# Optimization experiments

Hardware: AMD Instinct MI355X
Metric: run time of the kernel (lower is better)

Reference implementation:

```python
import jax, jax.numpy as jnp
import numpy as np

# UMAP a,b fitted offline for spread=5, min_dist=0.001 (curve_fit of 1/(1+a x^(2b)))
ALPHA = 0.1520
BETA = 0.7900
N_NODES = 50000
IN_DIM = 128
HID = 64
OUT_DIM = 2
N_EDGES = 800000


def setup_inputs() -> dict:
    key = jax.random.key(0)
    ks = jax.random.split(key, 8)
    feats = jax.random.normal(ks[0], (N_NODES, IN_DIM), dtype=jnp.float32)
    W1 = jax.random.normal(ks[1], (IN_DIM, HID), dtype=jnp.float32) / np.sqrt(IN_DIM)
    b1 = jnp.zeros((HID,), dtype=jnp.float32)
    W2 = jax.random.normal(ks[2], (HID, OUT_DIM), dtype=jnp.float32) / np.sqrt(HID)
    b2 = jnp.zeros((OUT_DIM,), dtype=jnp.float32)
    edge_index = jax.random.randint(ks[3], (2, N_EDGES), 0, N_NODES, dtype=jnp.int64)
    row_neg = jax.random.randint(ks[4], (N_EDGES,), 0, N_NODES, dtype=jnp.int64)
    col_neg = jax.random.randint(ks[5], (N_EDGES,), 0, N_NODES, dtype=jnp.int64)
    return {"features": feats, "W1": W1, "b1": b1, "W2": W2, "b2": b2,
            "edge_index": edge_index, "row_neg": row_neg, "col_neg": col_neg}


def _gcn_norm(edge_index, n_nodes):
    # add self-loops, symmetric normalization D^-1/2 (A+I) D^-1/2
    loops = jnp.arange(n_nodes, dtype=edge_index.dtype)
    row = jnp.concatenate([edge_index[0], loops])
    col = jnp.concatenate([edge_index[1], loops])
    deg = jax.ops.segment_sum(jnp.ones_like(row, dtype=jnp.float32), row,
                              num_segments=n_nodes)
    dinv = jnp.where(deg > 0, jax.lax.rsqrt(deg), 0.0)
    norm = dinv[row] * dinv[col]  # [E + N]
    return row, col, norm


def _gcn_conv(x, W, b, row, col, norm, n_nodes):
    h = x @ W                      # [N, out]
    msg = h[col] * norm[:, None]   # edge-indexed gather (irregular access)
    agg = jax.ops.segment_sum(msg, row, num_segments=n_nodes)
    return agg + b


def _forward(features, W1, b1, W2, b2, edge_index, row_neg, col_neg):
    n = features.shape[0]
    row, col, norm = _gcn_norm(edge_index, n)
    h = jax.nn.relu(_gcn_conv(features, W1, b1, row, col, norm, n))
    emb = _gcn_conv(h, W2, b2, row, col, norm, n)  # [N, 2]
    # pairwise L2 distances at positive edges and negative samples
    pos_diff = emb[edge_index[0]] - emb[edge_index[1]]
    neg_diff = emb[row_neg] - emb[col_neg]
    eps = 1e-12  # guards grad at zero distance (torch.norm subgradient is 0 there)
    pos_d = jnp.sqrt(jnp.sum(pos_diff * pos_diff, axis=1) + eps)
    neg_d = jnp.sqrt(jnp.sum(neg_diff * neg_diff, axis=1) + eps)
    lowdim_dist = jnp.concatenate([pos_d, neg_d], axis=0)  # [2E]
    q = 1.0 / (1.0 + ALPHA * jnp.power(lowdim_dist, 2.0 * BETA))
    return emb, q


def reference(features, W1, b1, W2, b2, edge_index, row_neg, col_neg):
    return _forward(features, W1, b1, W2, b2, edge_index, row_neg, col_neg)
```

## Files before the change

### kernel.cpp

```cpp
#include <hip/hip_runtime.h>
#include <hip/hip_fp16.h>
#include <math.h>

constexpr int   NN     = 50000;
constexpr int   IN_DIM = 128;
constexpr int   HID    = 64;
constexpr int   NE     = 800000;
constexpr float ALPHA  = 0.1520f;
constexpr float BETA   = 0.7900f;

constexpr int RSH = 7;
constexpr int RPB = 1 << RSH;
constexpr int NB  = (NN + RPB - 1) / RPB;
constexpr int NBP = 512;
constexpr int CH  = 4096;
constexpr int NCH = (NE + CH - 1) / CH;
constexpr int CAP = 4096;

__global__ __launch_bounds__(256) void k_bhist(const int* __restrict__ row,
                                               int* __restrict__ bpart) {
    __shared__ int h[NBP];
    int t = threadIdx.x;
    for (int i = t; i < NBP; i += 256) h[i] = 0;
    __syncthreads();
    int base = blockIdx.x * CH + t * 16;
    if (base + 15 < NE) {
        const int4* R = (const int4*)(row + base);
#pragma unroll
        for (int i = 0; i < 4; ++i) {
            int4 r = R[i];
            atomicAdd(&h[r.x >> RSH], 1);
            atomicAdd(&h[r.y >> RSH], 1);
            atomicAdd(&h[r.z >> RSH], 1);
            atomicAdd(&h[r.w >> RSH], 1);
        }
    } else {
        for (int i = 0; i < 16; ++i) {
            int e = base + i;
            if (e < NE) atomicAdd(&h[row[e] >> RSH], 1);
        }
    }
    __syncthreads();
    for (int b = t; b < NB; b += 256) bpart[b * NCH + blockIdx.x] = h[b];
}

__global__ __launch_bounds__(256) void k_bpre(int* __restrict__ bpart,
                                              int* __restrict__ bhist) {
    __shared__ int s[256];
    int b = blockIdx.x, t = threadIdx.x;
    int v = (t < NCH) ? bpart[b * NCH + t] : 0;
    s[t] = v;
    __syncthreads();
    for (int d = 1; d < 256; d <<= 1) {
        int u = (t >= d) ? s[t - d] : 0;
        __syncthreads();
        s[t] += u;
        __syncthreads();
    }
    if (t < NCH) bpart[b * NCH + t] = s[t] - v;
    if (t == 255) bhist[b] = s[255];
}

__global__ void k_bscan(const int* __restrict__ bhist, int* __restrict__ boffs) {
    __shared__ int s[NBP];
    int t = threadIdx.x;
    int v0 = (t < NB) ? bhist[t] : 0;
    int v1 = (t + 256 < NB) ? bhist[t + 256] : 0;
    s[t]       = v0;
    s[t + 256] = v1;
    __syncthreads();
    for (int d = 1; d < NBP; d <<= 1) {
        int u0 = (t >= d) ? s[t - d] : 0;
        int u1 = (t + 256 >= d) ? s[t + 256 - d] : 0;
        __syncthreads();
        s[t] += u0;
        s[t + 256] += u1;
        __syncthreads();
    }
    if (t < NB)       boffs[t]       = s[t] - v0;
    if (t + 256 < NB) boffs[t + 256] = s[t + 256] - v1;
    if (t == 0) boffs[NB] = NE;
}

__global__ __launch_bounds__(256) void k_binfill(const int* __restrict__ row,
                                                 const int* __restrict__ col,
                                                 const int* __restrict__ bpart,
                                                 const int* __restrict__ boffs,
                                                 unsigned int* __restrict__ bedge) {
    __shared__ int hist[NBP];
    __shared__ int scn[NBP];
    __shared__ int ebase[NB];
    __shared__ int gbase[NB];
    __shared__ int lcur[NB];
    __shared__ unsigned int pk[CH];
    __shared__ int gof[CH];

    int t = threadIdx.x;
    int base = blockIdx.x * CH + t * 16;
    int rw[16], cl[16];
    if (base + 15 < NE) {
        const int4* R = (const int4*)(row + base);
        const int4* C = (const int4*)(col + base);
#pragma unroll
        for (int i = 0; i < 4; ++i) {
            int4 r = R[i];
            int4 c = C[i];
            rw[4 * i + 0] = r.x; rw[4 * i + 1] = r.y; rw[4 * i + 2] = r.z; rw[4 * i + 3] = r.w;
            cl[4 * i + 0] = c.x; cl[4 * i + 1] = c.y; cl[4 * i + 2] = c.z; cl[4 * i + 3] = c.w;
        }
    } else {
        for (int i = 0; i < 16; ++i) {
            int e = base + i;
            if (e < NE) { rw[i] = row[e]; cl[i] = col[e]; } else rw[i] = -1;
        }
    }
    for (int i = t; i < NBP; i += 256) hist[i] = 0;
    __syncthreads();
#pragma unroll
    for (int i = 0; i < 16; ++i)
        if (rw[i] >= 0) atomicAdd(&hist[rw[i] >> RSH], 1);
    __syncthreads();
    scn[t] = hist[t];
    scn[t + 256] = hist[t + 256];
    __syncthreads();
    for (int d = 1; d < NBP; d <<= 1) {
        int v0 = (t >= d) ? scn[t - d] : 0;
        int v1 = (t + 256 >= d) ? scn[t + 256 - d] : 0;
        __syncthreads();
        scn[t] += v0;
        scn[t + 256] += v1;
        __syncthreads();
    }
    for (int b = t; b < NB; b += 256) {
        int h  = hist[b];
        int eb = scn[b] - h;
        ebase[b] = eb;
        lcur[b]  = eb;
        gbase[b] = boffs[b] + bpart[b * NCH + blockIdx.x];
    }
    __syncthreads();
#pragma unroll
    for (int i = 0; i < 16; ++i) {
        if (rw[i] >= 0) {
            int b = rw[i] >> RSH;
            int s = atomicAdd(&lcur[b], 1);
            pk[s]  = ((unsigned int)(rw[i] & (RPB - 1)) << 17) | (unsigned int)cl[i];
            gof[s] = gbase[b] + (s - ebase[b]);
        }
    }
    __syncthreads();
    int nval = min(CH, NE - blockIdx.x * CH);
    for (int s = t; s < nval; s += 256) bedge[gof[s]] = pk[s];
}

__global__ __launch_bounds__(256) void k_bucket(const unsigned int* __restrict__ bedge,
                                                const int* __restrict__ boffs,
                                                int* __restrict__ offs,
                                                float* __restrict__ dinv,
                                                int* __restrict__ scol) {
    __shared__ int cnt[RPB];
    __shared__ int loff[RPB];
    __shared__ int wtot[2];
    __shared__ unsigned int ld[CAP];
    __shared__ int buf[CAP];

    int b = blockIdx.x, t = threadIdx.x;
    int beg = boffs[b], end = boffs[b + 1];
    int m = end - beg;
    int nbase = b << RSH;

    if (t < RPB) cnt[t] = 0;
    __syncthreads();

    if (m <= CAP) {
        for (int i = t; i < m; i += 256) {
            unsigned int mm = bedge[beg + i];
            ld[i] = mm;
            atomicAdd(&cnt[mm >> 17], 1);
        }
        __syncthreads();
        if (t < RPB) {
            int v = cnt[t];
            int x = v;
#pragma unroll
            for (int d = 1; d < 64; d <<= 1) {
                int y = __shfl_up(x, d);
                if ((t & 63) >= d) x += y;
            }
            if ((t & 63) == 63) wtot[t >> 6] = x;
            loff[t] = x - v;
        }
        __syncthreads();
        if (t >= 64 && t < RPB) loff[t] += wtot[0];
        __syncthreads();
        if (t < RPB) {
            int n = nbase + t;
            if (n < NN) {
                offs[n] = beg + loff[t];
                dinv[n] = rsqrtf((float)(cnt[t] + 1));
            }
        }
        if (b == NB - 1 && t == 0) offs[NN] = NE;
        if (t < RPB) cnt[t] = loff[t];
        __syncthreads();
        for (int i = t; i < m; i += 256) {
            unsigned int mm = ld[i];
            int s = atomicAdd(&cnt[mm >> 17], 1);
            buf[s] = (int)(mm & 0x1FFFFu);
        }
        __syncthreads();
        for (int i = t; i < m; i += 256) scol[beg + i] = buf[i];
    } else {
        for (int i = t; i < m; i += 256)
            atomicAdd(&cnt[bedge[beg + i] >> 17], 1);
        __syncthreads();
        if (t < RPB) {
            int v = cnt[t];
            int x = v;
#pragma unroll
            for (int d = 1; d < 64; d <<= 1) {
                int y = __shfl_up(x, d);
                if ((t & 63) >= d) x += y;
            }
            if ((t & 63) == 63) wtot[t >> 6] = x;
            loff[t] = x - v;
        }
        __syncthreads();
        if (t >= 64 && t < RPB) loff[t] += wtot[0];
        __syncthreads();
        if (t < RPB) {
            int n = nbase + t;
            if (n < NN) {
                offs[n] = beg + loff[t];
                dinv[n] = rsqrtf((float)(cnt[t] + 1));
            }
        }
        if (b == NB - 1 && t == 0) offs[NN] = NE;
        if (t < RPB) cnt[t] = loff[t];
        __syncthreads();
        for (int i = t; i < m; i += 256) {
            unsigned int mm = bedge[beg + i];
            int s = atomicAdd(&cnt[mm >> 17], 1);
            scol[beg + s] = (int)(mm & 0x1FFFFu);
        }
    }
}

__global__ __launch_bounds__(256) void k_gemm1(const float* __restrict__ feat,
                                               const float* __restrict__ W1,
                                               const float* __restrict__ dinv,
                                               __half* __restrict__ h1s) {
    __shared__ float sW[IN_DIM * HID];
    __shared__ float sF[16][IN_DIM];
    int t = threadIdx.x;

    const float4* W4  = (const float4*)W1;
    float4*       sW4 = (float4*)sW;
#pragma unroll
    for (int i = 0; i < 8; ++i) sW4[t + i * 256] = W4[t + i * 256];

    int n0 = blockIdx.x * 16;
    const float4* F4  = (const float4*)(feat + (size_t)n0 * IN_DIM);
    float4*       sF4 = (float4*)&sF[0][0];
    sF4[t]       = F4[t];
    sF4[t + 256] = F4[t + 256];
    __syncthreads();

    int c = t & 63;
    int g = t >> 6;
    float acc[4] = {0.f, 0.f, 0.f, 0.f};
    for (int k = 0; k < IN_DIM; ++k) {
        float w = sW[k * HID + c];
#pragma unroll
        for (int i = 0; i < 4; ++i) acc[i] += sF[g * 4 + i][k] * w;
    }
#pragma unroll
    for (int i = 0; i < 4; ++i) {
        int n = n0 + g * 4 + i;
        h1s[(size_t)n * HID + c] = __float2half(acc[i] * dinv[n]);
    }
}

__global__ __launch_bounds__(256) void k_agg1(const int* __restrict__ offs,
                                              const int* __restrict__ scol,
                                              const float* __restrict__ dinv,
                                              const __half* __restrict__ h1s,
                                              const float* __restrict__ b1,
                                              const float* __restrict__ W2,
                                              float* __restrict__ h2s) {
    int n    = blockIdx.x * 4 + (threadIdx.x >> 6);
    int lane = threadIdx.x & 63;
    if (n >= NN) return;
    int g  = lane >> 4;
    int cq = lane & 15;
    int beg = offs[n], end = offs[n + 1];

    const uint2* H = (const uint2*)h1s;
    float a0 = 0.f, a1 = 0.f, a2 = 0.f, a3 = 0.f;
    int k = beg + g;
    for (; k + 12 < end; k += 16) {
        int c0 = scol[k], c1 = scol[k + 4], c2 = scol[k + 8], c3 = scol[k + 12];
        uint2 v0 = H[(size_t)c0 * 16 + cq];
        uint2 v1 = H[(size_t)c1 * 16 + cq];
        uint2 v2 = H[(size_t)c2 * 16 + cq];
        uint2 v3 = H[(size_t)c3 * 16 + cq];
        float2 f0a = __half22float2(*(__half2*)&v0.x), f0b = __half22float2(*(__half2*)&v0.y);
        float2 f1a = __half22float2(*(__half2*)&v1.x), f1b = __half22float2(*(__half2*)&v1.y);
        float2 f2a = __half22float2(*(__half2*)&v2.x), f2b = __half22float2(*(__half2*)&v2.y);
        float2 f3a = __half22float2(*(__half2*)&v3.x), f3b = __half22float2(*(__half2*)&v3.y);
        a0 += (f0a.x + f1a.x) + (f2a.x + f3a.x);
        a1 += (f0a.y + f1a.y) + (f2a.y + f3a.y);
        a2 += (f0b.x + f1b.x) + (f2b.x + f3b.x);
        a3 += (f0b.y + f1b.y) + (f2b.y + f3b.y);
    }
    for (; k < end; k += 4) {
        uint2 v = H[(size_t)scol[k] * 16 + cq];
        float2 fa = __half22float2(*(__half2*)&v.x);
        float2 fb = __half22float2(*(__half2*)&v.y);
        a0 += fa.x; a1 += fa.y; a2 += fb.x; a3 += fb.y;
    }
    a0 += __shfl_xor(a0, 16); a0 += __shfl_xor(a0, 32);
    a1 += __shfl_xor(a1, 16); a1 += __shfl_xor(a1, 32);
    a2 += __shfl_xor(a2, 16); a2 += __shfl_xor(a2, 32);
    a3 += __shfl_xor(a3, 16); a3 += __shfl_xor(a3, 32);

    uint2 sv = H[(size_t)n * 16 + cq];
    float2 s0 = __half22float2(*(__half2*)&sv.x);
    float2 s1 = __half22float2(*(__half2*)&sv.y);
    float di = dinv[n];
    float4 b14 = ((const float4*)b1)[cq];
    a0 = fmaxf(di * (a0 + s0.x) + b14.x, 0.f);
    a1 = fmaxf(di * (a1 + s0.y) + b14.y, 0.f);
    a2 = fmaxf(di * (a2 + s1.x) + b14.z, 0.f);
    a3 = fmaxf(di * (a3 + s1.y) + b14.w, 0.f);

    float4 w01 = ((const float4*)W2)[cq * 2];
    float4 w23 = ((const float4*)W2)[cq * 2 + 1];
    float p0 = a0 * w01.x + a1 * w01.z + a2 * w23.x + a3 * w23.z;
    float p1 = a0 * w01.y + a1 * w01.w + a2 * w23.y + a3 * w23.w;
#pragma unroll
    for (int d = 8; d >= 1; d >>= 1) {
        p0 += __shfl_xor(p0, d);
        p1 += __shfl_xor(p1, d);
    }
    if (lane == 0) {
        h2s[(size_t)n * 2 + 0] = di * p0;
        h2s[(size_t)n * 2 + 1] = di * p1;
    }
}

__global__ __launch_bounds__(256) void k_agg2(const int* __restrict__ offs,
                                              const int* __restrict__ scol,
                                              const float* __restrict__ dinv,
                                              const float* __restrict__ h2s,
                                              const float* __restrict__ b2,
                                              float* __restrict__ emb) {
    int wid  = threadIdx.x >> 6;
    int lane = threadIdx.x & 63;
    int n = blockIdx.x * 16 + wid * 4 + (lane >> 4);
    int e = lane & 15;
    const float2* h22 = (const float2*)h2s;
    float e0 = 0.f, e1 = 0.f;
    int beg = 0, end = 0;
    if (n < NN) { beg = offs[n]; end = offs[n + 1]; }
    for (int k = beg + e; k < end; k += 16) {
        float2 v = h22[scol[k]];
        e0 += v.x;
        e1 += v.y;
    }
#pragma unroll
    for (int d = 8; d >= 1; d >>= 1) {
        e0 += __shfl_xor(e0, d);
        e1 += __shfl_xor(e1, d);
    }
    if (e == 0 && n < NN) {
        float di = dinv[n];
        float2 self = h22[n];
        emb[(size_t)n * 2 + 0] = di * (e0 + self.x) + b2[0];
        emb[(size_t)n * 2 + 1] = di * (e1 + self.y) + b2[1];
    }
}

__global__ void k_q(const int* __restrict__ pr, const int* __restrict__ pc,
                    const int* __restrict__ nr, const int* __restrict__ nc,
                    const float* __restrict__ emb, float* __restrict__ q) {
    int e = blockIdx.x * blockDim.x + threadIdx.x;
    if (e >= 2 * NE) return;
    int a, b;
    if (e < NE) { a = pr[e]; b = pc[e]; }
    else        { a = nr[e - NE]; b = nc[e - NE]; }
    const float2* e2 = (const float2*)emb;
    float2 A = e2[a], B = e2[b];
    float dx = A.x - B.x, dy = A.y - B.y;
    float d = sqrtf(dx * dx + dy * dy + 1e-12f);
    float p = exp2f(2.0f * BETA * log2f(d));
    q[e] = 1.0f / (1.0f + ALPHA * p);
}

extern "C" void kernel_launch(void* const* d_in, const int* in_sizes, int n_in,
                              void* d_out, int out_size, void* d_ws, size_t ws_size,
                              hipStream_t stream) {
    const float* feat = (const float*)d_in[0];
    const float* W1   = (const float*)d_in[1];
    const float* b1   = (const float*)d_in[2];
    const float* W2   = (const float*)d_in[3];
    const float* b2   = (const float*)d_in[4];
    const int*   ei   = (const int*)d_in[5];
    const int*   nrw  = (const int*)d_in[6];
    const int*   ncl  = (const int*)d_in[7];
    const int* row = ei;
    const int* col = ei + NE;

    char* cur = (char*)d_ws;
    auto alloc = [&](size_t bytes) -> char* {
        char* p = cur;
        cur += (bytes + 255) & ~(size_t)255;
        return p;
    };
    int*          bpart = (int*)alloc(sizeof(int) * (size_t)NB * NCH);
    int*          bhist = (int*)alloc(sizeof(int) * NB);
    int*          boffs = (int*)alloc(sizeof(int) * (NB + 1));
    int*          offs  = (int*)alloc(sizeof(int) * (NN + 1));
    float*        dinv  = (float*)alloc(sizeof(float) * NN);
    unsigned int* bedge = (unsigned int*)alloc(sizeof(unsigned int) * NE);
    int*          scol  = (int*)alloc(sizeof(int) * NE);
    float*        h2s   = (float*)alloc(sizeof(float) * (size_t)NN * 2);
    __half*       h1s   = (__half*)alloc(sizeof(__half) * (size_t)NN * HID);

    float* emb = (float*)d_out;
    float* q   = (float*)d_out + (size_t)NN * 2;

    k_bhist  <<<NCH, 256, 0, stream>>>(row, bpart);
    k_bpre   <<<NB, 256, 0, stream>>>(bpart, bhist);
    k_bscan  <<<1, 256, 0, stream>>>(bhist, boffs);
    k_binfill<<<NCH, 256, 0, stream>>>(row, col, bpart, boffs, bedge);
    k_bucket <<<NB, 256, 0, stream>>>(bedge, boffs, offs, dinv, scol);

    k_gemm1<<<NN / 16, 256, 0, stream>>>(feat, W1, dinv, h1s);

    k_agg1<<<(NN + 3) / 4, 256, 0, stream>>>(offs, scol, dinv, h1s, b1, W2, h2s);
    k_agg2<<<(NN + 15) / 16, 256, 0, stream>>>(offs, scol, dinv, h2s, b2, emb);

    k_q<<<(2 * NE + 255) / 256, 256, 0, stream>>>(row, col, nrw, ncl, emb, q);
}
```

Baseline: 104.9 us.

## Fold bucket scan into last-block pattern and fuse CSR bucketing with GEMM1

The separate block-prefix and global-scan kernels are merged into one kernel. The last block to finish, found through an atomic counter reset in k_bhist, runs the global bucket scan. The per-bucket CSR build kernel and the first feature GEMM are also fused: each bucket block computes dinv for its 128 nodes, then reuses its shared memory through a union to run the 128x64 GEMM over eight 16-row tiles. This removes two kernel launches and the inter-kernel gaps. In exchange the GEMM now runs on far fewer blocks, each working serially, so parallelism and memory-level concurrency for that stage drop.

```diff
diff --git a/kernel.cpp b/kernel.cpp
--- a/kernel.cpp
+++ b/kernel.cpp
@@ -18,7 +18,9 @@
 constexpr int CAP = 4096;
 
 __global__ __launch_bounds__(256) void k_bhist(const int* __restrict__ row,
-                                               int* __restrict__ bpart) {
+                                               int* __restrict__ bpart,
+                                               int* __restrict__ done) {
+    if (blockIdx.x == 0 && threadIdx.x == 0) *done = 0;
     __shared__ int h[NBP];
     int t = threadIdx.x;
     for (int i = t; i < NBP; i += 256) h[i] = 0;
@@ -44,9 +46,12 @@
     for (int b = t; b < NB; b += 256) bpart[b * NCH + blockIdx.x] = h[b];
 }
 
-__global__ __launch_bounds__(256) void k_bpre(int* __restrict__ bpart,
-                                              int* __restrict__ bhist) {
-    __shared__ int s[256];
+__global__ __launch_bounds__(256) void k_scan(int* __restrict__ bpart,
+                                              int* __restrict__ bhist,
+                                              int* __restrict__ boffs,
+                                              int* __restrict__ done) {
+    __shared__ int s[NBP];
+    __shared__ int isLast;
     int b = blockIdx.x, t = threadIdx.x;
     int v = (t < NCH) ? bpart[b * NCH + t] : 0;
     s[t] = v;
@@ -58,14 +63,18 @@
         __syncthreads();
     }
     if (t < NCH) bpart[b * NCH + t] = s[t] - v;
-    if (t == 255) bhist[b] = s[255];
-}
-
-__global__ void k_bscan(const int* __restrict__ bhist, int* __restrict__ boffs) {
-    __shared__ int s[NBP];
-    int t = threadIdx.x;
-    int v0 = (t < NB) ? bhist[t] : 0;
-    int v1 = (t + 256 < NB) ? bhist[t + 256] : 0;
+    if (t == 255)
+        __hip_atomic_store(&bhist[b], s[255], __ATOMIC_RELEASE, __HIP_MEMORY_SCOPE_AGENT);
+    __syncthreads();
+    if (t == 0) {
+        int prev = __hip_atomic_fetch_add(done, 1, __ATOMIC_ACQ_REL, __HIP_MEMORY_SCOPE_AGENT);
+        isLast = (prev == NB - 1);
+    }
+    __syncthreads();
+    if (!isLast) return;
+    int v0 = (t < NB) ? __hip_atomic_load(&bhist[t], __ATOMIC_ACQUIRE, __HIP_MEMORY_SCOPE_AGENT) : 0;
+    int v1 = (t + 256 < NB) ? __hip_atomic_load(&bhist[t + 256], __ATOMIC_ACQUIRE, __HIP_MEMORY_SCOPE_AGENT) : 0;
+    __syncthreads();
     s[t]       = v0;
     s[t + 256] = v1;
     __syncthreads();
@@ -153,131 +162,131 @@
     for (int s = t; s < nval; s += 256) bedge[gof[s]] = pk[s];
 }
 
-__global__ __launch_bounds__(256) void k_bucket(const unsigned int* __restrict__ bedge,
-                                                const int* __restrict__ boffs,
-                                                int* __restrict__ offs,
-                                                float* __restrict__ dinv,
-                                                int* __restrict__ scol) {
-    __shared__ int cnt[RPB];
-    __shared__ int loff[RPB];
-    __shared__ int wtot[2];
-    __shared__ unsigned int ld[CAP];
-    __shared__ int buf[CAP];
+__global__ __launch_bounds__(256) void k_bg(const unsigned int* __restrict__ bedge,
+                                            const int* __restrict__ boffs,
+                                            const float* __restrict__ feat,
+                                            const float* __restrict__ W1,
+                                            int* __restrict__ offs,
+                                            float* __restrict__ dinv,
+                                            int* __restrict__ scol,
+                                            __half* __restrict__ h1s) {
+    union SMem {
+        struct { int cnt[RPB]; int loff[RPB]; int wtot[2];
+                 unsigned int ld[CAP]; int buf[CAP]; } a;
+        struct { float sW[IN_DIM * HID]; float sF[16][IN_DIM]; } g;
+    };
+    __shared__ SMem sm;
 
     int b = blockIdx.x, t = threadIdx.x;
     int beg = boffs[b], end = boffs[b + 1];
     int m = end - beg;
     int nbase = b << RSH;
 
-    if (t < RPB) cnt[t] = 0;
-    __syncthreads();
-
+    if (t < RPB) sm.a.cnt[t] = 0;
+    __syncthreads();
     if (m <= CAP) {
         for (int i = t; i < m; i += 256) {
             unsigned int mm = bedge[beg + i];
-            ld[i] = mm;
-            atomicAdd(&cnt[mm >> 17], 1);
+            sm.a.ld[i] = mm;
+            atomicAdd(&sm.a.cnt[mm >> 17], 1);
         }
         __syncthreads();
         if (t < RPB) {
-            int v = cnt[t];
+            int v = sm.a.cnt[t];
             int x = v;
 #pragma unroll
             for (int d = 1; d < 64; d <<= 1) {
                 int y = __shfl_up(x, d);
                 if ((t & 63) >= d) x += y;
             }
-            if ((t & 63) == 63) wtot[t >> 6] = x;
-            loff[t] = x - v;
-        }
-        __syncthreads();
-        if (t >= 64 && t < RPB) loff[t] += wtot[0];
+            if ((t & 63) == 63) sm.a.wtot[t >> 6] = x;
+            sm.a.loff[t] = x - v;
+        }
+        __syncthreads();
+        if (t >= 64 && t < RPB) sm.a.loff[t] += sm.a.wtot[0];
         __syncthreads();
         if (t < RPB) {
             int n = nbase + t;
             if (n < NN) {
-                offs[n] = beg + loff[t];
-                dinv[n] = rsqrtf((float)(cnt[t] + 1));
+                offs[n] = beg + sm.a.loff[t];
+                dinv[n] = rsqrtf((float)(sm.a.cnt[t] + 1));
             }
         }
         if (b == NB - 1 && t == 0) offs[NN] = NE;
-        if (t < RPB) cnt[t] = loff[t];
+        if (t < RPB) sm.a.cnt[t] = sm.a.loff[t];
         __syncthreads();
         for (int i = t; i < m; i += 256) {
-            unsigned int mm = ld[i];
-            int s = atomicAdd(&cnt[mm >> 17], 1);
-            buf[s] = (int)(mm & 0x1FFFFu);
-        }
-        __syncthreads();
-        for (int i = t; i < m; i += 256) scol[beg + i] = buf[i];
+            unsigned int mm = sm.a.ld[i];
+            int s = atomicAdd(&sm.a.cnt[mm >> 17], 1);
+            sm.a.buf[s] = (int)(mm & 0x1FFFFu);
+        }
+        __syncthreads();
+        for (int i = t; i < m; i += 256) scol[beg + i] = sm.a.buf[i];
     } else {
         for (int i = t; i < m; i += 256)
-            atomicAdd(&cnt[bedge[beg + i] >> 17], 1);
+            atomicAdd(&sm.a.cnt[bedge[beg + i] >> 17], 1);
         __syncthreads();
         if (t < RPB) {
-            int v = cnt[t];
+            int v = sm.a.cnt[t];
             int x = v;
 #pragma unroll
             for (int d = 1; d < 64; d <<= 1) {
                 int y = __shfl_up(x, d);
                 if ((t & 63) >= d) x += y;
             }
-            if ((t & 63) == 63) wtot[t >> 6] = x;
-            loff[t] = x - v;
-        }
-        __syncthreads();
-        if (t >= 64 && t < RPB) loff[t] += wtot[0];
+            if ((t & 63) == 63) sm.a.wtot[t >> 6] = x;
+            sm.a.loff[t] = x - v;
+        }
+        __syncthreads();
+        if (t >= 64 && t < RPB) sm.a.loff[t] += sm.a.wtot[0];
         __syncthreads();
         if (t < RPB) {
             int n = nbase + t;
             if (n < NN) {
-                offs[n] = beg + loff[t];
-                dinv[n] = rsqrtf((float)(cnt[t] + 1));
+                offs[n] = beg + sm.a.loff[t];
+                dinv[n] = rsqrtf((float)(sm.a.cnt[t] + 1));
             }
         }
         if (b == NB - 1 && t == 0) offs[NN] = NE;
-        if (t < RPB) cnt[t] = loff[t];
+        if (t < RPB) sm.a.cnt[t] = sm.a.loff[t];
         __syncthreads();
         for (int i = t; i < m; i += 256) {
             unsigned int mm = bedge[beg + i];
-            int s = atomicAdd(&cnt[mm >> 17], 1);
+            int s = atomicAdd(&sm.a.cnt[mm >> 17], 1);
             scol[beg + s] = (int)(mm & 0x1FFFFu);
         }
     }
-}
-
-__global__ __launch_bounds__(256) void k_gemm1(const float* __restrict__ feat,
-                                               const float* __restrict__ W1,
-                                               const float* __restrict__ dinv,
-                                               __half* __restrict__ h1s) {
-    __shared__ float sW[IN_DIM * HID];
-    __shared__ float sF[16][IN_DIM];
-    int t = threadIdx.x;
-
-    const float4* W4  = (const float4*)W1;
-    float4*       sW4 = (float4*)sW;
-#pragma unroll
-    for (int i = 0; i < 8; ++i) sW4[t + i * 256] = W4[t + i * 256];
-
-    int n0 = blockIdx.x * 16;
-    const float4* F4  = (const float4*)(feat + (size_t)n0 * IN_DIM);
-    float4*       sF4 = (float4*)&sF[0][0];
-    sF4[t]       = F4[t];
-    sF4[t + 256] = F4[t + 256];
-    __syncthreads();
-
-    int c = t & 63;
-    int g = t >> 6;
-    float acc[4] = {0.f, 0.f, 0.f, 0.f};
-    for (int k = 0; k < IN_DIM; ++k) {
-        float w = sW[k * HID + c];
-#pragma unroll
-        for (int i = 0; i < 4; ++i) acc[i] += sF[g * 4 + i][k] * w;
-    }
-#pragma unroll
-    for (int i = 0; i < 4; ++i) {
-        int n = n0 + g * 4 + i;
-        h1s[(size_t)n * HID + c] = __float2half(acc[i] * dinv[n]);
+    __syncthreads();
+
+    {
+        const float4* W4  = (const float4*)W1;
+        float4*       sW4 = (float4*)sm.g.sW;
+#pragma unroll
+        for (int i = 0; i < 8; ++i) sW4[t + i * 256] = W4[t + i * 256];
+
+        for (int s8 = 0; s8 < 8; ++s8) {
+            int n0 = nbase + s8 * 16;
+            if (n0 >= NN) break;
+            __syncthreads();
+            const float4* F4  = (const float4*)(feat + (size_t)n0 * IN_DIM);
+            float4*       sF4 = (float4*)&sm.g.sF[0][0];
+            sF4[t]       = F4[t];
+            sF4[t + 256] = F4[t + 256];
+            __syncthreads();
+            int c = t & 63;
+            int g = t >> 6;
+            float acc[4] = {0.f, 0.f, 0.f, 0.f};
+            for (int k = 0; k < IN_DIM; ++k) {
+                float w = sm.g.sW[k * HID + c];
+#pragma unroll
+                for (int i = 0; i < 4; ++i) acc[i] += sm.g.sF[g * 4 + i][k] * w;
+            }
+#pragma unroll
+            for (int i = 0; i < 4; ++i) {
+                int n = n0 + g * 4 + i;
+                h1s[(size_t)n * HID + c] = __float2half(acc[i] * dinv[n]);
+            }
+        }
     }
 }
 
@@ -426,17 +435,15 @@
     int*          scol  = (int*)alloc(sizeof(int) * NE);
     float*        h2s   = (float*)alloc(sizeof(float) * (size_t)NN * 2);
     __half*       h1s   = (__half*)alloc(sizeof(__half) * (size_t)NN * HID);
+    int*          done  = (int*)alloc(sizeof(int) * 64);
 
     float* emb = (float*)d_out;
     float* q   = (float*)d_out + (size_t)NN * 2;
 
-    k_bhist  <<<NCH, 256, 0, stream>>>(row, bpart);
-    k_bpre   <<<NB, 256, 0, stream>>>(bpart, bhist);
-    k_bscan  <<<1, 256, 0, stream>>>(bhist, boffs);
+    k_bhist  <<<NCH, 256, 0, stream>>>(row, bpart, done);
+    k_scan   <<<NB, 256, 0, stream>>>(bpart, bhist, boffs, done);
     k_binfill<<<NCH, 256, 0, stream>>>(row, col, bpart, boffs, bedge);
-    k_bucket <<<NB, 256, 0, stream>>>(bedge, boffs, offs, dinv, scol);
-
-    k_gemm1<<<NN / 16, 256, 0, stream>>>(feat, W1, dinv, h1s);
+    k_bg     <<<NB, 256, 0, stream>>>(bedge, boffs, feat, W1, offs, dinv, scol, h1s);
 
     k_agg1<<<(NN + 3) / 4, 256, 0, stream>>>(offs, scol, dinv, h1s, b1, W2, h2s);
     k_agg2<<<(NN + 15) / 16, 256, 0, stream>>>(offs, scol, dinv, h2s, b2, emb);
```

Result: slower. 136.2 us (+29.8%).
